# Kernel optimization log

Measured on AMD Instinct MI355X. Metric: run time of the kernel, lower is better.

The kernel has to match this reference:

```python
import jax, jax.numpy as jnp
import numpy as np

B, N, DIM = 16, 4096, 1024   # batch, n_out query tokens, embedding dim
T, E = 8, 64                 # n_tasks (readout heads), per-task output channels


def setup_inputs() -> dict:
    key = jax.random.key(0)
    k1, k2, k3, k4 = jax.random.split(key, 4)
    output_embs = jax.random.normal(k1, (B, N, DIM), dtype=jnp.float32)
    output_readout_index = jax.random.randint(k2, (B, N), 0, T, dtype=jnp.int64)
    # Stacked per-task nn.Linear(dim, E) weights/biases (torch Linear: y = x @ W.T + b)
    bound = 1.0 / np.sqrt(DIM)
    W = jax.random.uniform(k3, (T, DIM, E), minval=-bound, maxval=bound, dtype=jnp.float32)
    b = jax.random.uniform(k4, (T, E), minval=-bound, maxval=bound, dtype=jnp.float32)
    return {"output_embs": output_embs, "output_readout_index": output_readout_index,
            "W": W, "b": b}


def reference(output_embs, output_readout_index, W, b):
    """Per-token head-selected linear readout.

    Equivalent to the torch module's per-task mask/gather/Linear loop: every
    token t with output_readout_index==k gets projections[k](emb_t). The torch
    version concatenates selected rows into a dict per task; here we keep the
    rows in dense token order [B, N, E] (same values, fixed shapes for jit).
    """
    # All-head projection: [B, N, T, E]
    all_out = jnp.einsum('bnd,tde->bnte', output_embs, W) + b
    # Select each token's assigned head
    idx = output_readout_index[..., None, None]          # [B, N, 1, 1]
    out = jnp.take_along_axis(all_out, idx, axis=2)[:, :, 0, :]  # [B, N, E]
    return out
```

## Files before the change

### kernel.cpp

```cpp
#include <hip/hip_runtime.h>
#include <hip/hip_bf16.h>

#define NTOK  65536
#define DIM_  1024
#define NHEAD 8
#define EOUT  64
#define KBLK  32
#define CNT_STRIDE 32

#define CH_ROWB   512
#define CH_LDS    (32 * CH_ROWB)
#define NCHUNK    8
#define NBUF      3

typedef __bf16 bf16x8 __attribute__((ext_vector_type(8)));
typedef float  f32x4  __attribute__((ext_vector_type(4)));
typedef unsigned short u16x8 __attribute__((ext_vector_type(8)));

__device__ inline __bf16 cvt_bf16(float f) {
    __hip_bfloat16 h = __float2bfloat16(f);
    return __builtin_bit_cast(__bf16, h);
}

__device__ inline void gload_lds16(const void* g, void* lds) {
    __builtin_amdgcn_global_load_lds(
        (const __attribute__((address_space(1))) unsigned int*)g,
        (__attribute__((address_space(3))) unsigned int*)lds,
        16, 0, 0);
}

__global__ __launch_bounds__(256) void pack_and_bucket(
    const float* __restrict__ W, const int* __restrict__ idx,
    unsigned short* __restrict__ Wp, int* __restrict__ cnt,
    int* __restrict__ list)
{
    int x = blockIdx.x * blockDim.x + threadIdx.x;
    {
        int j  = x & 7;
        int l  = (x >> 3) & 63;
        int et = (x >> 9) & 3;
        int kb = (x >> 11) & 31;
        int t  = x >> 16;
        int k = kb * 32 + (l >> 4) * 8 + j;
        int e = et * 16 + (l & 15);
        float v = W[((size_t)t * DIM_ + k) * EOUT + e];
        __hip_bfloat16 h = __float2bfloat16(v);
        Wp[x] = __builtin_bit_cast(unsigned short, h);
    }

    if (blockIdx.x < NTOK / 1024) {
        int wave = threadIdx.x >> 6;
        int lane = threadIdx.x & 63;
        int gw   = blockIdx.x * 4 + wave;
        int tbase = gw * 256;
        int t[4];
        #pragma unroll
        for (int c = 0; c < 4; ++c) t[c] = idx[tbase + c * 64 + lane];

        #pragma unroll
        for (int h = 0; h < NHEAD; ++h) {
            unsigned long long m[4];
            int nh = 0;
            #pragma unroll
            for (int c = 0; c < 4; ++c) {
                m[c] = __ballot(t[c] == h);
                nh += __popcll(m[c]);
            }
            int base = 0;
            if (lane == 0 && nh) base = atomicAdd(&cnt[h * CNT_STRIDE], nh);
            base = __shfl(base, 0, 64);
            int pre = 0;
            #pragma unroll
            for (int c = 0; c < 4; ++c) {
                if (t[c] == h) {
                    int rank = __popcll(m[c] & ((1ull << lane) - 1ull));
                    list[h * NTOK + base + pre + rank] = tbase + c * 64 + lane;
                }
                pre += __popcll(m[c]);
            }
        }
    }
}

__global__ __launch_bounds__(256, 3) void readout_gemm(
    const float* __restrict__ emb, const float* __restrict__ bias,
    const int* __restrict__ cnt, const int* __restrict__ list,
    const unsigned short* __restrict__ Wp, float* __restrict__ out)
{
    __shared__ __align__(16) char smem[NBUF * CH_LDS];

    int g = blockIdx.x;
    int head = -1, tile = 0, count = 0, total = 0;
    #pragma unroll
    for (int h = 0; h < NHEAD; ++h) {
        int c = cnt[h * CNT_STRIDE];
        int th = (c + 31) >> 5;
        if (head < 0 && g < total + th) { head = h; tile = g - total; count = c; }
        total += th;
    }
    if (head < 0) return;

    int wave = threadIdx.x >> 6;
    int lane = threadIdx.x & 63;
    int quad = lane >> 4, l16 = lane & 15;
    int rg = wave >> 1;
    int ep = wave & 1;
    int eb = ep * 2;

    const int* mylist = list + head * NTOK;
    int mbase = tile * 32;

    const char* gsrc[4];
    int u31 = lane & 31;
    #pragma unroll
    for (int i = 0; i < 4; ++i) {
        int row = wave * 8 + i * 2 + (lane >> 5);
        int m = mbase + row; if (m > count - 1) m = count - 1;
        gsrc[i] = (const char*)(emb + (size_t)mylist[m] * DIM_)
                  + ((u31 ^ (row & 15)) * 16);
    }
    char* ldsw = smem + (wave * 8) * CH_ROWB;

    int arow = rg * 16 + l16;

    const u16x8* wp = reinterpret_cast<const u16x8*>(Wp + (size_t)head * 65536);

    #pragma unroll
    for (int s = 0; s < 2; ++s) {
        char* d = ldsw + s * CH_LDS;
        #pragma unroll
        for (int i = 0; i < 4; ++i)
            gload_lds16(gsrc[i] + s * CH_ROWB, d + i * 1024);
    }

    f32x4 acc[2] = {};

    #pragma unroll
    for (int c = 0; c < NCHUNK; ++c) {
        asm volatile("s_waitcnt lgkmcnt(0)" ::: "memory");
        __builtin_amdgcn_s_barrier();
        if (c + 2 < NCHUNK) {
            char* d = ldsw + ((c + 2) % NBUF) * CH_LDS;
            #pragma unroll
            for (int i = 0; i < 4; ++i)
                gload_lds16(gsrc[i] + (c + 2) * CH_ROWB, d + i * 1024);
        }
        if (c < NCHUNK - 2)       asm volatile("s_waitcnt vmcnt(8)" ::: "memory");
        else if (c == NCHUNK - 2) asm volatile("s_waitcnt vmcnt(4)" ::: "memory");
        else                      asm volatile("s_waitcnt vmcnt(0)" ::: "memory");
        __builtin_amdgcn_s_barrier();

        const char* bb = smem + (c % NBUF) * CH_LDS + arow * CH_ROWB;
        #pragma unroll
        for (int kb = 0; kb < 4; ++kb) {
            int u0 = kb * 8 + quad * 2;
            f32x4 lo = *(const f32x4*)(bb + (((u0 + 0) ^ l16) * 16));
            f32x4 hi = *(const f32x4*)(bb + (((u0 + 1) ^ l16) * 16));
            u16x8 b0 = wp[((c * 4 + kb) * 4 + eb + 0) * 64 + lane];
            u16x8 b1 = wp[((c * 4 + kb) * 4 + eb + 1) * 64 + lane];
            bf16x8 a;
            #pragma unroll
            for (int j = 0; j < 4; ++j) {
                a[j]     = cvt_bf16(lo[j]);
                a[j + 4] = cvt_bf16(hi[j]);
            }
            acc[0] = __builtin_amdgcn_mfma_f32_16x16x32_bf16(
                a, __builtin_bit_cast(bf16x8, b0), acc[0], 0, 0, 0);
            acc[1] = __builtin_amdgcn_mfma_f32_16x16x32_bf16(
                a, __builtin_bit_cast(bf16x8, b1), acc[1], 0, 0, 0);
        }
    }

    int tok[4];
    #pragma unroll
    for (int i = 0; i < 4; ++i) {
        int m = mbase + rg * 16 + quad * 4 + i;
        tok[i] = (m < count) ? mylist[m] : -1;
    }
    #pragma unroll
    for (int e = 0; e < 2; ++e) {
        float bv = bias[head * EOUT + (eb + e) * 16 + l16];
        #pragma unroll
        for (int i = 0; i < 4; ++i)
            if (tok[i] >= 0)
                __builtin_nontemporal_store(acc[e][i] + bv,
                    &out[(size_t)tok[i] * EOUT + (eb + e) * 16 + l16]);
    }
}

extern "C" void kernel_launch(void* const* d_in, const int* in_sizes, int n_in,
                              void* d_out, int out_size, void* d_ws, size_t ws_size,
                              hipStream_t stream) {
    const float* emb  = (const float*)d_in[0];
    const int*   idx  = (const int*)d_in[1];
    const float* W    = (const float*)d_in[2];
    const float* bias = (const float*)d_in[3];
    float* out = (float*)d_out;

    char* ws = (char*)d_ws;
    int* cnt  = (int*)ws;
    int* list = (int*)(ws + 1024);
    unsigned short* Wp = (unsigned short*)(ws + 1024 + (size_t)NHEAD * NTOK * sizeof(int));

    (void)hipMemsetAsync(cnt, 0, NHEAD * CNT_STRIDE * sizeof(int), stream);
    pack_and_bucket<<<(NHEAD * KBLK * 4 * 64 * 8) / 256, 256, 0, stream>>>(W, idx, Wp, cnt, list);
    readout_gemm<<<2055, 256, 0, stream>>>(emb, bias, cnt, list, Wp, out);
}
```

Baseline: 406.0 us.

## Restructure GEMM into larger double-buffered chunks and vectorize weight packing via LDS

The readout GEMM now streams 1 KB row chunks in 4 double-buffered stages instead of 512 B chunks in 8 triple-buffered stages. It also hoists each chunk's weight-fragment loads into registers ahead of the next prefetch, and occupancy drops to 2 blocks per CU to fit the 64 KB LDS footprint. The weight pack kernel now uses one block per 32x64 weight tile: it stages the tile through LDS and writes 16-byte vectors, replacing the strided per-element scatter and cutting the launch from 2048 blocks to 256. The aim is to cut barrier and loop overhead and make weight packing coalesced. The risk is fewer bytes in flight per CU for the memory-bound embedding stream, plus higher register pressure from the hoisted B fragments.

```diff
diff --git a/kernel.cpp b/kernel.cpp
--- a/kernel.cpp
+++ b/kernel.cpp
@@ -8,10 +8,10 @@
 #define KBLK  32
 #define CNT_STRIDE 32
 
-#define CH_ROWB   512
+#define CH_ROWB   1024
 #define CH_LDS    (32 * CH_ROWB)
-#define NCHUNK    8
-#define NBUF      3
+#define NCHUNK    4
+#define NBUF      2
 
 typedef __bf16 bf16x8 __attribute__((ext_vector_type(8)));
 typedef float  f32x4  __attribute__((ext_vector_type(4)));
@@ -34,24 +34,33 @@
     unsigned short* __restrict__ Wp, int* __restrict__ cnt,
     int* __restrict__ list)
 {
-    int x = blockIdx.x * blockDim.x + threadIdx.x;
+    __shared__ float lw[2048];
+    int b   = blockIdx.x;
+    int tid = threadIdx.x;
+
+    const f32x4* src = reinterpret_cast<const f32x4*>(W + (size_t)b * 2048);
+    f32x4 v0 = src[tid * 2];
+    f32x4 v1 = src[tid * 2 + 1];
+    *reinterpret_cast<f32x4*>(&lw[tid * 8])     = v0;
+    *reinterpret_cast<f32x4*>(&lw[tid * 8 + 4]) = v1;
+    __syncthreads();
+
     {
-        int j  = x & 7;
-        int l  = (x >> 3) & 63;
-        int et = (x >> 9) & 3;
-        int kb = (x >> 11) & 31;
-        int t  = x >> 16;
-        int k = kb * 32 + (l >> 4) * 8 + j;
-        int e = et * 16 + (l & 15);
-        float v = W[((size_t)t * DIM_ + k) * EOUT + e];
-        __hip_bfloat16 h = __float2bfloat16(v);
-        Wp[x] = __builtin_bit_cast(unsigned short, h);
-    }
-
-    if (blockIdx.x < NTOK / 1024) {
-        int wave = threadIdx.x >> 6;
-        int lane = threadIdx.x & 63;
-        int gw   = blockIdx.x * 4 + wave;
+        int et = tid >> 6, l = tid & 63;
+        u16x8 o;
+        #pragma unroll
+        for (int j = 0; j < 8; ++j) {
+            float v = lw[((l >> 4) * 8 + j) * 64 + et * 16 + (l & 15)];
+            __hip_bfloat16 h = __float2bfloat16(v);
+            o[j] = __builtin_bit_cast(unsigned short, h);
+        }
+        *reinterpret_cast<u16x8*>(Wp + (size_t)b * 2048 + tid * 8) = o;
+    }
+
+    if (b < NTOK / 1024) {
+        int wave = tid >> 6;
+        int lane = tid & 63;
+        int gw   = b * 4 + wave;
         int tbase = gw * 256;
         int t[4];
         #pragma unroll
@@ -82,7 +91,7 @@
     }
 }
 
-__global__ __launch_bounds__(256, 3) void readout_gemm(
+__global__ __launch_bounds__(256, 2) void readout_gemm(
     const float* __restrict__ emb, const float* __restrict__ bias,
     const int* __restrict__ cnt, const int* __restrict__ list,
     const unsigned short* __restrict__ Wp, float* __restrict__ out)
@@ -110,54 +119,53 @@
     const int* mylist = list + head * NTOK;
     int mbase = tile * 32;
 
-    const char* gsrc[4];
-    int u31 = lane & 31;
-    #pragma unroll
-    for (int i = 0; i < 4; ++i) {
-        int row = wave * 8 + i * 2 + (lane >> 5);
+    const char* gsrc[8];
+    #pragma unroll
+    for (int i = 0; i < 8; ++i) {
+        int row = wave * 8 + i;
         int m = mbase + row; if (m > count - 1) m = count - 1;
         gsrc[i] = (const char*)(emb + (size_t)mylist[m] * DIM_)
-                  + ((u31 ^ (row & 15)) * 16);
-    }
-    char* ldsw = smem + (wave * 8) * CH_ROWB;
+                  + ((lane ^ (row & 15)) * 16);
+    }
+    char* ldsw = smem + (size_t)(wave * 8) * CH_ROWB;
 
     int arow = rg * 16 + l16;
 
     const u16x8* wp = reinterpret_cast<const u16x8*>(Wp + (size_t)head * 65536);
 
     #pragma unroll
-    for (int s = 0; s < 2; ++s) {
-        char* d = ldsw + s * CH_LDS;
-        #pragma unroll
-        for (int i = 0; i < 4; ++i)
-            gload_lds16(gsrc[i] + s * CH_ROWB, d + i * 1024);
-    }
+    for (int i = 0; i < 8; ++i)
+        gload_lds16(gsrc[i], ldsw + i * CH_ROWB);
 
     f32x4 acc[2] = {};
+    u16x8 B[8][2];
 
     #pragma unroll
     for (int c = 0; c < NCHUNK; ++c) {
         asm volatile("s_waitcnt lgkmcnt(0)" ::: "memory");
         __builtin_amdgcn_s_barrier();
-        if (c + 2 < NCHUNK) {
-            char* d = ldsw + ((c + 2) % NBUF) * CH_LDS;
-            #pragma unroll
-            for (int i = 0; i < 4; ++i)
-                gload_lds16(gsrc[i] + (c + 2) * CH_ROWB, d + i * 1024);
-        }
-        if (c < NCHUNK - 2)       asm volatile("s_waitcnt vmcnt(8)" ::: "memory");
-        else if (c == NCHUNK - 2) asm volatile("s_waitcnt vmcnt(4)" ::: "memory");
-        else                      asm volatile("s_waitcnt vmcnt(0)" ::: "memory");
+
+        #pragma unroll
+        for (int kb = 0; kb < 8; ++kb) {
+            B[kb][0] = wp[((c * 8 + kb) * 4 + eb + 0) * 64 + lane];
+            B[kb][1] = wp[((c * 8 + kb) * 4 + eb + 1) * 64 + lane];
+        }
+        if (c + 1 < NCHUNK) {
+            char* d = ldsw + ((c + 1) & 1) * CH_LDS;
+            #pragma unroll
+            for (int i = 0; i < 8; ++i)
+                gload_lds16(gsrc[i] + (c + 1) * CH_ROWB, d + i * CH_ROWB);
+        }
+        if (c + 1 < NCHUNK) asm volatile("s_waitcnt vmcnt(8)" ::: "memory");
+        else                asm volatile("s_waitcnt vmcnt(0)" ::: "memory");
         __builtin_amdgcn_s_barrier();
 
-        const char* bb = smem + (c % NBUF) * CH_LDS + arow * CH_ROWB;
-        #pragma unroll
-        for (int kb = 0; kb < 4; ++kb) {
+        const char* bb = smem + (c & 1) * CH_LDS + (size_t)arow * CH_ROWB;
+        #pragma unroll
+        for (int kb = 0; kb < 8; ++kb) {
             int u0 = kb * 8 + quad * 2;
             f32x4 lo = *(const f32x4*)(bb + (((u0 + 0) ^ l16) * 16));
             f32x4 hi = *(const f32x4*)(bb + (((u0 + 1) ^ l16) * 16));
-            u16x8 b0 = wp[((c * 4 + kb) * 4 + eb + 0) * 64 + lane];
-            u16x8 b1 = wp[((c * 4 + kb) * 4 + eb + 1) * 64 + lane];
             bf16x8 a;
             #pragma unroll
             for (int j = 0; j < 4; ++j) {
@@ -165,9 +173,9 @@
                 a[j + 4] = cvt_bf16(hi[j]);
             }
             acc[0] = __builtin_amdgcn_mfma_f32_16x16x32_bf16(
-                a, __builtin_bit_cast(bf16x8, b0), acc[0], 0, 0, 0);
+                a, __builtin_bit_cast(bf16x8, B[kb][0]), acc[0], 0, 0, 0);
             acc[1] = __builtin_amdgcn_mfma_f32_16x16x32_bf16(
-                a, __builtin_bit_cast(bf16x8, b1), acc[1], 0, 0, 0);
+                a, __builtin_bit_cast(bf16x8, B[kb][1]), acc[1], 0, 0, 0);
         }
     }
 
@@ -203,6 +211,6 @@
     unsigned short* Wp = (unsigned short*)(ws + 1024 + (size_t)NHEAD * NTOK * sizeof(int));
 
     (void)hipMemsetAsync(cnt, 0, NHEAD * CNT_STRIDE * sizeof(int), stream);
-    pack_and_bucket<<<(NHEAD * KBLK * 4 * 64 * 8) / 256, 256, 0, stream>>>(W, idx, Wp, cnt, list);
+    pack_and_bucket<<<256, 256, 0, stream>>>(W, idx, Wp, cnt, list);
     readout_gemm<<<2055, 256, 0, stream>>>(emb, bias, cnt, list, Wp, out);
 }
```

Measured after the change: 398.2 us. Within noise of the previous version (-1.9%).
